# Performance work log

Measured on AMD Instinct MI355X. Metric: run time of the kernel, lower is better.

Reference implementation:

```python
import jax, jax.numpy as jnp
import numpy as np

KS = 7            # kernel_size
DIL = 1           # dilatation
H = 96
W = 96
PAD = DIL * (KS - 1) // 2
SHIFTS = [s * DIL for s in range(KS)]


def stack_kernel(a, axis=-2):
    # a: [B, H+2*PAD, W+2*PAD, C] -> [B, H, W, ks^2, C] (or stacked on `axis`)
    return jnp.stack([a[:, y:H + y, x:W + x] for y in SHIFTS for x in SHIFTS], axis=axis)


def make_padding_mask():
    # zeros inside, -inf in the halo; stacked per window position -> [1,H,W,ks^2]
    z = jnp.pad(jnp.zeros((1, H, W, 1), jnp.float32),
                ((0, 0), (PAD, PAD), (PAD, PAD), (0, 0)),
                constant_values=-jnp.inf)
    return stack_kernel(z, axis=-1)[..., 0, :]  # [1,H,W,ks^2]


def setup_inputs() -> dict:
    key = jax.random.key(0)
    ks = jax.random.split(key, 8)
    B, C, KD, OD = 2, 128, 64, 128
    Q = jax.random.normal(ks[0], (B, H, W, C), jnp.float32)
    K = jax.random.normal(ks[1], (B, H, W, C), jnp.float32)
    V = jax.random.normal(ks[2], (B, H, W, C), jnp.float32)
    s = 1.0 / np.sqrt(C)
    Wq = jax.random.normal(ks[3], (C, KD), jnp.float32) * s
    Wk = jax.random.normal(ks[4], (C, KD), jnp.float32) * s
    Wv = jax.random.normal(ks[5], (C, OD), jnp.float32) * s
    return {"Q": Q, "K": K, "V": V,
            "Wq": Wq, "bq": jnp.zeros((KD,), jnp.float32),
            "Wk": Wk, "bk": jnp.zeros((KD,), jnp.float32),
            "Wv": Wv, "bv": jnp.zeros((OD,), jnp.float32)}


def reference(Q, K, V, Wq, bq, Wk, bk, Wv, bv):
    # Dense projections (key_dim is not None)
    q = Q @ Wq + bq                      # [B,H,W,KD]
    k = K @ Wk + bk                      # [B,H,W,KD]
    Dk = jnp.asarray(q.shape[-1], q.dtype)

    pad4 = ((0, 0), (PAD, PAD), (PAD, PAD), (0, 0))
    k_stk = stack_kernel(jnp.pad(k, pad4), axis=-2)   # [B,H,W,ks^2,KD]
    mask = make_padding_mask()                        # [1,H,W,ks^2]

    # w = Q . K_neighbors + padding mask; softmax over ks^2 window
    w = jnp.einsum('bhwd,bhwkd->bhwk', q, k_stk) + mask
    scores = jax.nn.softmax(w / jnp.sqrt(Dk), axis=-1)  # [B,H,W,ks^2]

    v_stk = stack_kernel(jnp.pad(V, pad4), axis=-2)   # [B,H,W,ks^2,E]
    out = jnp.einsum('bhwk,bhwke->bhwe', scores, v_stk)
    # V_d Dense with relu (out_dim is not None)
    out = jax.nn.relu(out @ Wv + bv)                  # [B,H,W,out_dim]
    return out
```

## Files before the change

kernel.cpp:

```cpp
#include <hip/hip_runtime.h>
#include <math.h>

#define BH 2
#define HH 96
#define WW 96
#define NPIX (BH*HH*WW)

#define TH 8
#define TW 4
#define NH 140

#define NEGBIG (-3.0e38f)

typedef __attribute__((ext_vector_type(8))) short short8;
typedef __attribute__((ext_vector_type(4))) float f32x4;

__device__ __forceinline__ unsigned short f2bf(float f) {
    union { float f; unsigned u; } a; a.f = f;
    return (unsigned short)((a.u + 0x7FFFu + ((a.u >> 16) & 1u)) >> 16);
}
__device__ __forceinline__ unsigned packbf(float lo, float hi) {
    return (unsigned)f2bf(lo) | ((unsigned)f2bf(hi) << 16);
}

#define WT_STRIDE 136

__global__ __launch_bounds__(256) void prep_proj_kernel(
    const float* __restrict__ Qg, const float* __restrict__ Kg,
    const float* __restrict__ Wq, const float* __restrict__ bq,
    const float* __restrict__ Wk, const float* __restrict__ bk,
    const float* __restrict__ Wv,
    unsigned short* __restrict__ q_bf, unsigned short* __restrict__ k_bf,
    unsigned short* __restrict__ WvT)
{
    __shared__ unsigned short WT[64 * WT_STRIDE];
    const int bid = blockIdx.x;
    const int tid = threadIdx.x;

    if (bid < 576) {
        const bool isq = bid < 288;
        const float* __restrict__ X   = isq ? Qg : Kg;
        const float* __restrict__ Wt  = isq ? Wq : Wk;
        const float* __restrict__ bia = isq ? bq : bk;
        unsigned short* __restrict__ Y = isq ? q_bf : k_bf;

        {
            const float4* __restrict__ W4 = reinterpret_cast<const float4*>(Wt);
            #pragma unroll
            for (int i = 0; i < 8; ++i) {
                const int e  = tid + 256 * i;
                const int k  = e >> 4;
                const int n4 = (e & 15) * 4;
                const float4 v = W4[e];
                WT[(n4 + 0) * WT_STRIDE + k] = f2bf(v.x);
                WT[(n4 + 1) * WT_STRIDE + k] = f2bf(v.y);
                WT[(n4 + 2) * WT_STRIDE + k] = f2bf(v.z);
                WT[(n4 + 3) * WT_STRIDE + k] = f2bf(v.w);
            }
        }
        __syncthreads();

        const int lane = tid & 63;
        const int wvv  = tid >> 6;
        const int row0 = ((bid % 288) * 4 + wvv) * 16;
        const int qd = lane >> 4, m = lane & 15;

        short8 afr[4];
        #pragma unroll
        for (int ks = 0; ks < 4; ++ks) {
            const float4* __restrict__ src = reinterpret_cast<const float4*>(
                X + (size_t)(row0 + m) * 128 + ks * 32 + qd * 8);
            const float4 a0 = src[0], a1 = src[1];
            short8 f;
            f[0] = (short)f2bf(a0.x); f[1] = (short)f2bf(a0.y);
            f[2] = (short)f2bf(a0.z); f[3] = (short)f2bf(a0.w);
            f[4] = (short)f2bf(a1.x); f[5] = (short)f2bf(a1.y);
            f[6] = (short)f2bf(a1.z); f[7] = (short)f2bf(a1.w);
            afr[ks] = f;
        }

        #pragma unroll
        for (int n = 0; n < 4; ++n) {
            f32x4 acc = {};
            #pragma unroll
            for (int ks = 0; ks < 4; ++ks) {
                const short8 bfr = *reinterpret_cast<const short8*>(
                    &WT[(n * 16 + m) * WT_STRIDE + ks * 32 + qd * 8]);
                acc = __builtin_amdgcn_mfma_f32_16x16x32_bf16(afr[ks], bfr, acc, 0, 0, 0);
            }
            const int col = n * 16 + m;
            const float bb = bia[col];
            #pragma unroll
            for (int r = 0; r < 4; ++r)
                Y[(size_t)(row0 + qd * 4 + r) * 64 + col] = f2bf(acc[r] + bb);
        }
    } else {
        const int base = (bid - 576) * 1024 + tid * 4;
        #pragma unroll
        for (int i = 0; i < 4; ++i) {
            const int e = base + i;
            WvT[e] = f2bf(Wv[(e & 127) * 128 + (e >> 7)]);
        }
    }
}

#define PS_OFF 0
#define PS_STRIDE 168
#define AS_OFF 5376
#define AS_STRIDE 136
#define SM_OFF 9728
#define V_OFF 10240
#define VS 160
#define LDS_N 30720

__global__ __launch_bounds__(512, 4) void attn_kernel(
    const unsigned short* __restrict__ q_bf, const unsigned short* __restrict__ k_bf,
    const float* __restrict__ V, const unsigned short* __restrict__ WvT,
    const float* __restrict__ bv, float* __restrict__ out)
{
    __shared__ unsigned short lds[LDS_N];
    const int tid  = threadIdx.x;
    const int lane = tid & 63;
    const int wv   = tid >> 6;
    const int mt   = wv & 1;
    const int ng   = wv >> 1;

    const int bid  = blockIdx.x;
    const int bimg = bid / 288;
    const int tidx = bid % 288;
    const int ty = tidx / 24, tx = tidx % 24;
    const int y0 = ty * TH, x0 = tx * TW;

    const int qd = lane >> 4, m = lane & 15;

    float* __restrict__ smf = reinterpret_cast<float*>(&lds[SM_OFF]);

    {
        const int q4  = tid & 31;
        const int pp0 = tid >> 5;
        const int fsw = (q4 >> 1) & 7;
        unsigned* __restrict__ vl32 = reinterpret_cast<unsigned*>(&lds[V_OFF]);
        #pragma unroll
        for (int rnd = 0; rnd < 5; ++rnd) {
            const int pp  = rnd * 16 + pp0;
            const int p0p = pp * 2;
            int o0, o1;
            {
                const int hy = (p0p * 6554) >> 16;
                const int hx = p0p - hy * 10;
                const int iy = y0 - 3 + hy, ix = x0 - 3 + hx;
                const bool ok = ((unsigned)iy < HH) & ((unsigned)ix < WW) & (p0p < NH);
                o0 = ok ? ((bimg * HH + iy) * WW + ix) : 0;
            }
            {
                const int p1p = p0p + 1;
                const int hy = (p1p * 6554) >> 16;
                const int hx = p1p - hy * 10;
                const int iy = y0 - 3 + hy, ix = x0 - 3 + hx;
                const bool ok = ((unsigned)iy < HH) & ((unsigned)ix < WW) & (p1p < NH);
                o1 = ok ? ((bimg * HH + iy) * WW + ix) : 0;
            }
            const float4 a = *reinterpret_cast<const float4*>(V + (size_t)o0 * 128 + q4 * 4);
            const float4 b = *reinterpret_cast<const float4*>(V + (size_t)o1 * 128 + q4 * 4);
            const int pb   = rnd * 4 + (pp0 >> 2);
            const int sb   = pb ^ ((pb < 16) ? fsw : (fsw & 3));
            const int colw = sb * 4 + (pp & 3);
            const int rb   = q4 * 4;
            vl32[(rb + 0) * (VS / 2) + colw] = packbf(a.x, b.x);
            vl32[(rb + 1) * (VS / 2) + colw] = packbf(a.y, b.y);
            vl32[(rb + 2) * (VS / 2) + colw] = packbf(a.z, b.z);
            vl32[(rb + 3) * (VS / 2) + colw] = packbf(a.w, b.w);
        }
    }

    short8 qa[2];
    {
        const int py = mt * 4 + (m >> 2), px = m & 3;
        const size_t gq = (size_t)(bimg * HH + y0 + py) * WW + (x0 + px);
        #pragma unroll
        for (int ks = 0; ks < 2; ++ks)
            qa[ks] = *reinterpret_cast<const short8*>(q_bf + gq * 64 + ks * 32 + qd * 8);
    }

    const int ntbase = (ng < 2) ? ng * 3 : 6 + (ng - 2) * 2;
    const int ntcnt  = (ng < 2) ? 3 : 2;

    f32x4 sc[3];
    #pragma unroll
    for (int n5 = 0; n5 < 3; ++n5) {
        if (n5 >= ntcnt) break;
        const int h  = (ntbase + n5) * 16 + m;
        const int hy = (h * 6554) >> 16;
        const int hx = h - hy * 10;
        const int iy = y0 - 3 + hy, ix = x0 - 3 + hx;
        const bool ok = ((unsigned)iy < HH) & ((unsigned)ix < WW) & (h < NH);
        const size_t ob = ok ? (size_t)((bimg * HH + iy) * WW + ix) * 64 : 0;
        f32x4 a = {};
        #pragma unroll
        for (int ks = 0; ks < 2; ++ks) {
            const short8 bfr = *reinterpret_cast<const short8*>(k_bf + ob + ks * 32 + qd * 8);
            a = __builtin_amdgcn_mfma_f32_16x16x32_bf16(qa[ks], bfr, a, 0, 0, 0);
        }
        sc[n5] = a;
    }

    float sm[4] = {0.f, 0.f, 0.f, 0.f};
    #pragma unroll
    for (int n5 = 0; n5 < 3; ++n5) {
        if (n5 >= ntcnt) break;
        const int h  = (ntbase + n5) * 16 + m;
        const int hy = (h * 6554) >> 16;
        const int hx = h - hy * 10;
        const int iy = y0 - 3 + hy, ix = x0 - 3 + hx;
        const bool imgok = ((unsigned)iy < HH) & ((unsigned)ix < WW) & (h < NH);
        const int py = mt * 4 + qd;
        const int col = (ntbase + n5) * 16 + m;
        #pragma unroll
        for (int r = 0; r < 4; ++r) {
            const bool ok = imgok & ((unsigned)(hy - py) <= 6u) & ((unsigned)(hx - r) <= 6u);
            const float e = ok ? __expf(sc[n5][r] * 0.125f) : 0.f;
            sm[r] += e;
            const int row = mt * 16 + qd * 4 + r;
            lds[PS_OFF + row * PS_STRIDE + col] = f2bf(e);
        }
    }
    #pragma unroll
    for (int r = 0; r < 4; ++r)
        #pragma unroll
        for (int off = 1; off < 16; off <<= 1)
            sm[r] += __shfl_xor(sm[r], off);

    if (m == 0) {
        #pragma unroll
        for (int r = 0; r < 4; ++r) {
            const int row = mt * 16 + qd * 4 + r;
            smf[row * 4 + ng] = sm[r];
        }
    }
    __syncthreads();

    float fac[4];
    #pragma unroll
    for (int r = 0; r < 4; ++r) {
        const int row = mt * 16 + qd * 4 + r;
        const float S = smf[row * 4 + 0] + smf[row * 4 + 1]
                      + smf[row * 4 + 2] + smf[row * 4 + 3];
        fac[r] = 1.0f / S;
    }

    short8 wf[2][4];
    #pragma unroll
    for (int n2 = 0; n2 < 2; ++n2)
        #pragma unroll
        for (int ks = 0; ks < 4; ++ks)
            wf[n2][ks] = *reinterpret_cast<const short8*>(
                WvT + ((ng * 2 + n2) * 16 + m) * 128 + ks * 32 + qd * 8);

    short8 pa[5];
    #pragma unroll
    for (int ks = 0; ks < 5; ++ks)
        pa[ks] = *reinterpret_cast<const short8*>(
            &lds[PS_OFF + (mt * 16 + m) * PS_STRIDE + ks * 32 + qd * 8]);

    f32x4 oacc[2] = {};
    #pragma unroll
    for (int ks = 0; ks < 5; ++ks) {
        const int kb = ks * 4 + qd;
        #pragma unroll
        for (int n2 = 0; n2 < 2; ++n2) {
            const int ch = (ng * 2 + n2) * 16 + m;
            const int f  = (ch >> 3) & 7;
            const int sb = kb ^ ((kb < 16) ? f : (f & 3));
            const short8 bfr = *reinterpret_cast<const short8*>(
                &lds[V_OFF + ch * VS + sb * 8]);
            oacc[n2] = __builtin_amdgcn_mfma_f32_16x16x32_bf16(pa[ks], bfr, oacc[n2], 0, 0, 0);
        }
    }

    #pragma unroll
    for (int n2 = 0; n2 < 2; ++n2)
        #pragma unroll
        for (int r = 0; r < 4; ++r) {
            const int row = mt * 16 + qd * 4 + r;
            const int col = (ng * 2 + n2) * 16 + m;
            lds[AS_OFF + row * AS_STRIDE + col] = f2bf(oacc[n2][r] * fac[r]);
        }
    __syncthreads();

    short8 aa[4];
    #pragma unroll
    for (int ks = 0; ks < 4; ++ks)
        aa[ks] = *reinterpret_cast<const short8*>(
            &lds[AS_OFF + (mt * 16 + m) * AS_STRIDE + ks * 32 + qd * 8]);

    #pragma unroll
    for (int n2 = 0; n2 < 2; ++n2) {
        const int nt = ng * 2 + n2;
        f32x4 a = {};
        #pragma unroll
        for (int ks = 0; ks < 4; ++ks)
            a = __builtin_amdgcn_mfma_f32_16x16x32_bf16(aa[ks], wf[n2][ks], a, 0, 0, 0);
        const int col = nt * 16 + m;
        const float bb = bv[col];
        #pragma unroll
        for (int r = 0; r < 4; ++r) {
            const int py = mt * 4 + qd, px = r;
            const size_t gp = (size_t)(bimg * HH + y0 + py) * WW + (x0 + px);
            out[gp * 128 + col] = fmaxf(a[r] + bb, 0.f);
        }
    }
}

extern "C" void kernel_launch(void* const* d_in, const int* in_sizes, int n_in,
                              void* d_out, int out_size, void* d_ws, size_t ws_size,
                              hipStream_t stream)
{
    const float* Q  = (const float*)d_in[0];
    const float* K  = (const float*)d_in[1];
    const float* V  = (const float*)d_in[2];
    const float* Wq = (const float*)d_in[3];
    const float* bq = (const float*)d_in[4];
    const float* bk = (const float*)d_in[6];
    const float* Wk = (const float*)d_in[5];
    const float* Wv = (const float*)d_in[7];
    const float* bv = (const float*)d_in[8];
    float* out = (float*)d_out;

    unsigned short* wbase = (unsigned short*)d_ws;
    unsigned short* WvT   = wbase + 16384;
    unsigned short* q_bf  = wbase + 32768;
    unsigned short* k_bf  = q_bf + (size_t)NPIX * 64;

    prep_proj_kernel<<<592, 256, 0, stream>>>(Q, K, Wq, bq, Wk, bk, Wv,
                                              q_bf, k_bf, WvT);
    attn_kernel<<<576, 512, 0, stream>>>(q_bf, k_bf, V, WvT, bv, out);
}
```

Before: 109.5 us.

## Fuse Q/K projections into attention kernel with LDS-resident halo keys

Drops the separate projection pass that wrote bf16 q and k to global memory. The attention kernel now projects its own tile's queries and its 140-pixel key halo directly from the fp32 inputs using MFMA, and stores the results in LDS. A tiny kernel only transposes and converts the three weight matrices. This removes the global round trip for q/k and one full kernel's worth of work, but recomputes the halo keys per tile (about 4.4x redundancy) and raises LDS use, which may lower occupancy.

Result: slower. 123.8 us (+13.1%).

```diff
diff --git a/kernel.cpp b/kernel.cpp
--- a/kernel.cpp
+++ b/kernel.cpp
@@ -10,8 +10,6 @@
 #define TW 4
 #define NH 140
 
-#define NEGBIG (-3.0e38f)
-
 typedef __attribute__((ext_vector_type(8))) short short8;
 typedef __attribute__((ext_vector_type(4))) float f32x4;
 
@@ -23,99 +21,46 @@
     return (unsigned)f2bf(lo) | ((unsigned)f2bf(hi) << 16);
 }
 
-#define WT_STRIDE 136
-
-__global__ __launch_bounds__(256) void prep_proj_kernel(
-    const float* __restrict__ Qg, const float* __restrict__ Kg,
-    const float* __restrict__ Wq, const float* __restrict__ bq,
-    const float* __restrict__ Wk, const float* __restrict__ bk,
+__global__ __launch_bounds__(256) void wprep_kernel(
+    const float* __restrict__ Wq, const float* __restrict__ Wk,
     const float* __restrict__ Wv,
-    unsigned short* __restrict__ q_bf, unsigned short* __restrict__ k_bf,
+    unsigned short* __restrict__ WqT, unsigned short* __restrict__ WkT,
     unsigned short* __restrict__ WvT)
 {
-    __shared__ unsigned short WT[64 * WT_STRIDE];
-    const int bid = blockIdx.x;
-    const int tid = threadIdx.x;
-
-    if (bid < 576) {
-        const bool isq = bid < 288;
-        const float* __restrict__ X   = isq ? Qg : Kg;
-        const float* __restrict__ Wt  = isq ? Wq : Wk;
-        const float* __restrict__ bia = isq ? bq : bk;
-        unsigned short* __restrict__ Y = isq ? q_bf : k_bf;
-
-        {
-            const float4* __restrict__ W4 = reinterpret_cast<const float4*>(Wt);
-            #pragma unroll
-            for (int i = 0; i < 8; ++i) {
-                const int e  = tid + 256 * i;
-                const int k  = e >> 4;
-                const int n4 = (e & 15) * 4;
-                const float4 v = W4[e];
-                WT[(n4 + 0) * WT_STRIDE + k] = f2bf(v.x);
-                WT[(n4 + 1) * WT_STRIDE + k] = f2bf(v.y);
-                WT[(n4 + 2) * WT_STRIDE + k] = f2bf(v.z);
-                WT[(n4 + 3) * WT_STRIDE + k] = f2bf(v.w);
-            }
-        }
-        __syncthreads();
-
-        const int lane = tid & 63;
-        const int wvv  = tid >> 6;
-        const int row0 = ((bid % 288) * 4 + wvv) * 16;
-        const int qd = lane >> 4, m = lane & 15;
-
-        short8 afr[4];
-        #pragma unroll
-        for (int ks = 0; ks < 4; ++ks) {
-            const float4* __restrict__ src = reinterpret_cast<const float4*>(
-                X + (size_t)(row0 + m) * 128 + ks * 32 + qd * 8);
-            const float4 a0 = src[0], a1 = src[1];
-            short8 f;
-            f[0] = (short)f2bf(a0.x); f[1] = (short)f2bf(a0.y);
-            f[2] = (short)f2bf(a0.z); f[3] = (short)f2bf(a0.w);
-            f[4] = (short)f2bf(a1.x); f[5] = (short)f2bf(a1.y);
-            f[6] = (short)f2bf(a1.z); f[7] = (short)f2bf(a1.w);
-            afr[ks] = f;
-        }
-
-        #pragma unroll
-        for (int n = 0; n < 4; ++n) {
-            f32x4 acc = {};
-            #pragma unroll
-            for (int ks = 0; ks < 4; ++ks) {
-                const short8 bfr = *reinterpret_cast<const short8*>(
-                    &WT[(n * 16 + m) * WT_STRIDE + ks * 32 + qd * 8]);
-                acc = __builtin_amdgcn_mfma_f32_16x16x32_bf16(afr[ks], bfr, acc, 0, 0, 0);
-            }
-            const int col = n * 16 + m;
-            const float bb = bia[col];
-            #pragma unroll
-            for (int r = 0; r < 4; ++r)
-                Y[(size_t)(row0 + qd * 4 + r) * 64 + col] = f2bf(acc[r] + bb);
-        }
-    } else {
-        const int base = (bid - 576) * 1024 + tid * 4;
-        #pragma unroll
-        for (int i = 0; i < 4; ++i) {
-            const int e = base + i;
-            WvT[e] = f2bf(Wv[(e & 127) * 128 + (e >> 7)]);
-        }
-    }
-}
-
-#define PS_OFF 0
+    const int base = (blockIdx.x * 256 + threadIdx.x) * 4;
+    #pragma unroll
+    for (int i = 0; i < 4; ++i) {
+        const int e = base + i;
+        if (e < 8192) {
+            WqT[e] = f2bf(Wq[(e & 127) * 64 + (e >> 7)]);
+        } else if (e < 16384) {
+            const int e2 = e - 8192;
+            WkT[e2] = f2bf(Wk[(e2 & 127) * 64 + (e2 >> 7)]);
+        } else {
+            const int e3 = e - 16384;
+            WvT[e3] = f2bf(Wv[(e3 & 127) * 128 + (e3 >> 7)]);
+        }
+    }
+}
+
+#define KH_OFF 0
+#define KH_STRIDE 72
+#define QH_ROW 160
+#define AS_OFF 0
+#define AS_STRIDE 136
+#define PS_OFF 13824
 #define PS_STRIDE 168
-#define AS_OFF 5376
-#define AS_STRIDE 136
-#define SM_OFF 9728
-#define V_OFF 10240
+#define SM_OFF 19200
+#define V_OFF 19456
 #define VS 160
-#define LDS_N 30720
+#define LDS_N 39936
 
 __global__ __launch_bounds__(512, 4) void attn_kernel(
-    const unsigned short* __restrict__ q_bf, const unsigned short* __restrict__ k_bf,
-    const float* __restrict__ V, const unsigned short* __restrict__ WvT,
+    const float* __restrict__ Qg, const float* __restrict__ Kg,
+    const float* __restrict__ V,
+    const unsigned short* __restrict__ WqT, const unsigned short* __restrict__ WkT,
+    const unsigned short* __restrict__ WvT,
+    const float* __restrict__ bq, const float* __restrict__ bk,
     const float* __restrict__ bv, float* __restrict__ out)
 {
     __shared__ unsigned short lds[LDS_N];
@@ -173,14 +118,66 @@
         }
     }
 
+    {
+        const int nunits = (wv < 4) ? 2 : 1;
+        #pragma unroll
+        for (int ui = 0; ui < 2; ++ui) {
+            if (ui >= nunits) break;
+            const int u   = (ui == 0) ? wv : (8 + wv);
+            const bool isq = (u >= 10);
+            int o;
+            if (!isq) {
+                const int p  = u * 16 + m;
+                const int hy = (p * 6554) >> 16;
+                const int hx = p - hy * 10;
+                const int iy = y0 - 3 + hy, ix = x0 - 3 + hx;
+                const bool ok = ((unsigned)iy < HH) & ((unsigned)ix < WW) & (p < NH);
+                o = ok ? ((bimg * HH + iy) * WW + ix) : 0;
+            } else {
+                const int tp = (u - 10) * 16 + m;
+                o = (bimg * HH + y0 + (tp >> 2)) * WW + x0 + (tp & 3);
+            }
+            const float* __restrict__ Xs = isq ? Qg : Kg;
+            short8 afr[4];
+            #pragma unroll
+            for (int ks = 0; ks < 4; ++ks) {
+                const float4* __restrict__ s4 = reinterpret_cast<const float4*>(
+                    Xs + (size_t)o * 128 + ks * 32 + qd * 8);
+                const float4 a0 = s4[0], a1 = s4[1];
+                short8 f;
+                f[0] = (short)f2bf(a0.x); f[1] = (short)f2bf(a0.y);
+                f[2] = (short)f2bf(a0.z); f[3] = (short)f2bf(a0.w);
+                f[4] = (short)f2bf(a1.x); f[5] = (short)f2bf(a1.y);
+                f[6] = (short)f2bf(a1.z); f[7] = (short)f2bf(a1.w);
+                afr[ks] = f;
+            }
+            const unsigned short* __restrict__ WT = isq ? WqT : WkT;
+            const float* __restrict__ bia = isq ? bq : bk;
+            const int rowbase = (!isq) ? u * 16 : (QH_ROW + (u - 10) * 16);
+            #pragma unroll
+            for (int n = 0; n < 4; ++n) {
+                f32x4 acc = {};
+                #pragma unroll
+                for (int ks = 0; ks < 4; ++ks) {
+                    const short8 bfr = *reinterpret_cast<const short8*>(
+                        WT + (n * 16 + m) * 128 + ks * 32 + qd * 8);
+                    acc = __builtin_amdgcn_mfma_f32_16x16x32_bf16(afr[ks], bfr, acc, 0, 0, 0);
+                }
+                const int col = n * 16 + m;
+                const float bb = bia[col];
+                #pragma unroll
+                for (int r = 0; r < 4; ++r)
+                    lds[KH_OFF + (rowbase + qd * 4 + r) * KH_STRIDE + col] = f2bf(acc[r] + bb);
+            }
+        }
+    }
+    __syncthreads();
+
     short8 qa[2];
-    {
-        const int py = mt * 4 + (m >> 2), px = m & 3;
-        const size_t gq = (size_t)(bimg * HH + y0 + py) * WW + (x0 + px);
-        #pragma unroll
-        for (int ks = 0; ks < 2; ++ks)
-            qa[ks] = *reinterpret_cast<const short8*>(q_bf + gq * 64 + ks * 32 + qd * 8);
-    }
+    #pragma unroll
+    for (int ks = 0; ks < 2; ++ks)
+        qa[ks] = *reinterpret_cast<const short8*>(
+            &lds[KH_OFF + (QH_ROW + mt * 16 + m) * KH_STRIDE + ks * 32 + qd * 8]);
 
     const int ntbase = (ng < 2) ? ng * 3 : 6 + (ng - 2) * 2;
     const int ntcnt  = (ng < 2) ? 3 : 2;
@@ -189,16 +186,12 @@
     #pragma unroll
     for (int n5 = 0; n5 < 3; ++n5) {
         if (n5 >= ntcnt) break;
-        const int h  = (ntbase + n5) * 16 + m;
-        const int hy = (h * 6554) >> 16;
-        const int hx = h - hy * 10;
-        const int iy = y0 - 3 + hy, ix = x0 - 3 + hx;
-        const bool ok = ((unsigned)iy < HH) & ((unsigned)ix < WW) & (h < NH);
-        const size_t ob = ok ? (size_t)((bimg * HH + iy) * WW + ix) * 64 : 0;
+        const int h = (ntbase + n5) * 16 + m;
         f32x4 a = {};
         #pragma unroll
         for (int ks = 0; ks < 2; ++ks) {
-            const short8 bfr = *reinterpret_cast<const short8*>(k_bf + ob + ks * 32 + qd * 8);
+            const short8 bfr = *reinterpret_cast<const short8*>(
+                &lds[KH_OFF + h * KH_STRIDE + ks * 32 + qd * 8]);
             a = __builtin_amdgcn_mfma_f32_16x16x32_bf16(qa[ks], bfr, a, 0, 0, 0);
         }
         sc[n5] = a;
@@ -320,18 +313,17 @@
     const float* V  = (const float*)d_in[2];
     const float* Wq = (const float*)d_in[3];
     const float* bq = (const float*)d_in[4];
+    const float* Wk = (const float*)d_in[5];
     const float* bk = (const float*)d_in[6];
-    const float* Wk = (const float*)d_in[5];
     const float* Wv = (const float*)d_in[7];
     const float* bv = (const float*)d_in[8];
     float* out = (float*)d_out;
 
     unsigned short* wbase = (unsigned short*)d_ws;
-    unsigned short* WvT   = wbase + 16384;
-    unsigned short* q_bf  = wbase + 32768;
-    unsigned short* k_bf  = q_bf + (size_t)NPIX * 64;
-
-    prep_proj_kernel<<<592, 256, 0, stream>>>(Q, K, Wq, bq, Wk, bk, Wv,
-                                              q_bf, k_bf, WvT);
-    attn_kernel<<<576, 512, 0, stream>>>(q_bf, k_bf, V, WvT, bv, out);
-}
+    unsigned short* WqT = wbase;
+    unsigned short* WkT = wbase + 8192;
+    unsigned short* WvT = wbase + 16384;
+
+    wprep_kernel<<<32, 256, 0, stream>>>(Wq, Wk, Wv, WqT, WkT, WvT);
+    attn_kernel<<<576, 512, 0, stream>>>(Q, K, V, WqT, WkT, WvT, bq, bk, bv, out);
+}
```
